# Optimization experiments

Hardware: AMD Instinct MI355X
Metric: run time of the kernel (lower is better)

## Reference

```python
import jax, jax.numpy as jnp
import numpy as np

K = 100
TEMPERATURE = 0.1


def setup_inputs() -> dict:
    key = jax.random.key(0)
    k1, k2 = jax.random.split(key)
    x = jax.random.normal(k1, (8, 128, 60, 60), dtype=jnp.float32)
    W = jax.random.normal(k2, (128, 2 * K), dtype=jnp.float32) * 0.02  # torch Linear(k*2, d_model).weight
    b = jnp.zeros((128,), dtype=jnp.float32)
    return {"x": x, "W": W, "b": b}


def reference(x, W, b):
    x0, x1 = jnp.split(x, 2, axis=0)
    n, c, h, w = x0.shape
    hw = h * w
    # n c h w -> n (h w) c
    f0 = jnp.transpose(x0.reshape(n, c, hw), (0, 2, 1))
    f1 = jnp.transpose(x1.reshape(n, c, hw), (0, 2, 1))
    # (f0/sqrt(c)) @ (f1/sqrt(c))^T / T  ==  f0 @ f1^T / (c*T)
    sm = jnp.einsum('nld,nsd->nls', f0, f1) / (c * TEMPERATURE)
    cm = (jax.nn.softmax(sm, axis=1) * jax.nn.softmax(sm, axis=2)).reshape(n, hw * hw)
    _, topi = jax.lax.top_k(cm, K)  # (n, K)
    qindex = topi // hw
    rindex = topi % hw
    coords0 = jnp.stack([qindex % w, qindex // w], axis=-1).astype(jnp.float32) / w  # (n, K, 2) as (x, y)
    coords1 = jnp.stack([rindex % w, rindex // w], axis=-1).astype(jnp.float32) / w
    # create_meshgrid(h, w, normalized=False): (1, h*w, 2) with (x, y), row-major
    gy, gx = jnp.meshgrid(jnp.arange(h), jnp.arange(w), indexing='ij')
    grid = jnp.stack([gx, gy], axis=-1).reshape(1, hw, 2).astype(jnp.float32) / w
    offsets0 = grid[:, :, None, :] - coords0[:, None, :, :]  # (n, hw, K, 2)
    offsets1 = grid[:, :, None, :] - coords1[:, None, :, :]
    emb0 = offsets0.reshape(n, hw, 2 * K) @ W.T + b  # (n, hw, d_model)
    emb1 = offsets1.reshape(n, hw, 2 * K) @ W.T + b
    f0 = f0 + emb0
    f1 = f1 + emb1
    f = jnp.concatenate([f0, f1], axis=0)  # (2n, hw, d)
    # n (h w) d -> n d h w
    return jnp.transpose(f, (0, 2, 1)).reshape(2 * n, c, h, w)
```

## Files before the change

### kernel.cpp

```cpp
#include <hip/hip_runtime.h>

#define HW 3600
#define PADR 3712
#define NF4 900
#define CAP 16384
#define KSEL 100
#define NT 58
typedef unsigned long long U64;

using short8   = __attribute__((ext_vector_type(8))) short;
using float4v  = __attribute__((ext_vector_type(4))) float;
using float16v = __attribute__((ext_vector_type(16))) float;

__device__ __forceinline__ unsigned monof(float f) {
    unsigned b = __float_as_uint(f);
    return (b & 0x80000000u) ? ~b : (b | 0x80000000u);
}
__device__ __forceinline__ float unmonof(unsigned m) {
    return __uint_as_float((m & 0x80000000u) ? (m ^ 0x80000000u) : ~m);
}
__device__ __forceinline__ unsigned short f2bf(float f) {
    unsigned b = __float_as_uint(f);
    return (unsigned short)((b + 0x7FFFu + ((b >> 16) & 1u)) >> 16);
}
__device__ __forceinline__ float bf2f(unsigned short h) {
    return __uint_as_float(((unsigned)h) << 16);
}
__device__ __forceinline__ void async16(const void* g, void* l) {
    __builtin_amdgcn_global_load_lds((const __attribute__((address_space(1))) void*)g,
                                     (__attribute__((address_space(3))) void*)l, 16, 0, 0);
}


__global__ __launch_bounds__(256) void conv_k(
    const float* __restrict__ x,
    unsigned short* __restrict__ hiT, unsigned short* __restrict__ loT)
{
    int b = blockIdx.z, l0 = blockIdx.x * 64, d0 = blockIdx.y * 64;
    __shared__ float t[64][65];
    int tid = threadIdx.x;
#pragma unroll
    for (int r = 0; r < 4; r++) {
        int idx = tid + 256 * r;
        int d = idx >> 4, lq = idx & 15;
        int l = l0 + lq * 4;
        const float* src = x + ((size_t)b * 128 + d0 + d) * HW;
        float4 v;
        if (l + 3 < HW) v = *(const float4*)(src + l);
        else {
            v.x = (l     < HW) ? src[l]     : 0.f;
            v.y = (l + 1 < HW) ? src[l + 1] : 0.f;
            v.z = (l + 2 < HW) ? src[l + 2] : 0.f;
            v.w = (l + 3 < HW) ? src[l + 3] : 0.f;
        }
        t[lq * 4 + 0][d] = v.x; t[lq * 4 + 1][d] = v.y;
        t[lq * 4 + 2][d] = v.z; t[lq * 4 + 3][d] = v.w;
    }
    __syncthreads();
    const int rblk = l0 >> 7;
#pragma unroll
    for (int r = 0; r < 2; r++) {
        int idx = tid + 256 * r;
        int l = idx & 63, dq = idx >> 6;
        unsigned hp[4], lp[4];
#pragma unroll
        for (int j = 0; j < 4; j++) {
            float f0 = t[l][dq * 8 + 2 * j], f1 = t[l][dq * 8 + 2 * j + 1];
            unsigned short h0 = f2bf(f0), h1 = f2bf(f1);
            unsigned short g0 = f2bf(f0 - bf2f(h0)), g1 = f2bf(f1 - bf2f(h1));
            hp[j] = (unsigned)h0 | ((unsigned)h1 << 16);
            lp[j] = (unsigned)g0 | ((unsigned)g1 << 16);
        }
        size_t o = ((size_t)(b * 29 + rblk) * 16 + (d0 >> 3) + dq) * 1024
                 + (size_t)((l0 + l) & 127) * 8;
        *(uint4*)(hiT + o) = make_uint4(hp[0], hp[1], hp[2], hp[3]);
        *(uint4*)(loT + o) = make_uint4(lp[0], lp[1], lp[2], lp[3]);
    }
}

__global__ __launch_bounds__(256) void gemm_mfma_k(
    const unsigned short* __restrict__ hiT, const unsigned short* __restrict__ loT,
    float* __restrict__ den_row, float* __restrict__ den_col,
    float* __restrict__ maxvt)
{
    const int batch = blockIdx.z, bx = blockIdx.x, by = blockIdx.y;
    __shared__ __align__(16) unsigned short stage[4][4][128][8];
    __shared__ float rowsumS[128], colsumS[128];

    const int tid = threadIdx.x;
    const int lane = tid & 63, w = tid >> 6;
    const int wr = w >> 1, wc = w & 1;
    const int l31 = lane & 31, h = lane >> 5;

    if (tid < 128) { rowsumS[tid] = 0.f; colsumS[tid] = 0.f; }

    const unsigned short* psrc = (w == 0) ? hiT : (w == 1) ? loT : (w == 2) ? hiT : loT;
    const int bsel = (w < 2) ? batch : batch + 4;
    const int rblk = (w < 2) ? by : bx;
    const size_t cbase = ((size_t)(bsel * 29 + rblk) * 16) * 1024;

    float16v acc[2][2];
#pragma unroll
    for (int i = 0; i < 2; i++)
#pragma unroll
        for (int j = 0; j < 2; j++) acc[i][j] = (float16v)(0.f);

    for (int k0 = 0; k0 < 128; k0 += 32) {
#pragma unroll
        for (int i = 0; i < 8; i++) {
            int kb = i >> 1, half = i & 1;
            const unsigned short* g = psrc + cbase + (size_t)((k0 >> 3) + kb) * 1024
                                    + (half << 9) + lane * 8;
            async16(g, &stage[w][kb][half << 6][0]);
        }
        __syncthreads();
#pragma unroll
        for (int j = 0; j < 2; j++) {
            int kb = j * 2 + h;
            short8 ah[2], al[2], bh[2], bl[2];
#pragma unroll
            for (int t = 0; t < 2; t++) {
                ah[t] = *(const short8*)&stage[0][kb][wr * 64 + t * 32 + l31][0];
                al[t] = *(const short8*)&stage[1][kb][wr * 64 + t * 32 + l31][0];
                bh[t] = *(const short8*)&stage[2][kb][wc * 64 + t * 32 + l31][0];
                bl[t] = *(const short8*)&stage[3][kb][wc * 64 + t * 32 + l31][0];
            }
#pragma unroll
            for (int mt = 0; mt < 2; mt++)
#pragma unroll
                for (int nt = 0; nt < 2; nt++) {
                    acc[mt][nt] = __builtin_amdgcn_mfma_f32_32x32x16_bf16(ah[mt], bh[nt], acc[mt][nt], 0, 0, 0);
                    acc[mt][nt] = __builtin_amdgcn_mfma_f32_32x32x16_bf16(ah[mt], bl[nt], acc[mt][nt], 0, 0, 0);
                    acc[mt][nt] = __builtin_amdgcn_mfma_f32_32x32x16_bf16(al[mt], bh[nt], acc[mt][nt], 0, 0, 0);
                }
        }
        __syncthreads();
    }

    const float scale = 0.078125f;
    float cs[2] = {0.f, 0.f};
    const int ct = bx * 2 + wc;
#pragma unroll
    for (int mt = 0; mt < 2; mt++) {
#pragma unroll
        for (int reg = 0; reg < 16; reg++) {
            int rloc = (reg & 3) + 8 * (reg >> 2) + 4 * h;
            int row128 = wr * 64 + mt * 32 + rloc;
            int l = by * 128 + row128;
            bool lv = (l < HW);
            float rs = 0.f, mx = -3.4e38f;
#pragma unroll
            for (int nt = 0; nt < 2; nt++) {
                int s = bx * 128 + wc * 64 + nt * 32 + l31;
                float v = acc[mt][nt][reg] * scale;
                if (s < HW) {
                    float e = __expf(v);
                    rs += e;
                    if (lv) cs[nt] += e;
                    mx = fmaxf(mx, v);
                }
            }
#pragma unroll
            for (int off = 1; off < 32; off <<= 1) {
                rs += __shfl_xor(rs, off);
                mx = fmaxf(mx, __shfl_xor(mx, off));
            }
            if (l31 == 0) {
                atomicAdd(&rowsumS[row128], rs);
                if (lv) maxvt[((size_t)batch * NT + ct) * PADR + l] = mx;
            }
        }
    }
#pragma unroll
    for (int nt = 0; nt < 2; nt++) {
        cs[nt] += __shfl_xor(cs[nt], 32);
        if (h == 0) atomicAdd(&colsumS[wc * 64 + nt * 32 + l31], cs[nt]);
    }
    __syncthreads();
    if (tid < 128) {
        int l = by * 128 + tid;
        if (l < HW) atomicAdd(&den_row[(size_t)batch * HW + l], rowsumS[tid]);
        int s = bx * 128 + tid;
        if (s < HW) atomicAdd(&den_col[(size_t)batch * HW + s], colsumS[tid]);
    }
}

__global__ __launch_bounds__(256) void logs_k(
    const float* __restrict__ den, float* __restrict__ lnD)
{
    int i = blockIdx.x * 256 + threadIdx.x;
    if (i < 28800) lnD[i] = __logf(den[i]);
}

__global__ __launch_bounds__(64) void tilestat_k(
    const float* __restrict__ lnDc, float* __restrict__ minlnc, float* __restrict__ maxlnc)
{
    int t = blockIdx.x, b = blockIdx.z, tid = threadIdx.x;
    int j = t * 64 + tid;
    float v = (j < HW) ? lnDc[(size_t)b * HW + j] : 0.f;
    float mn = (j < HW) ? v : 3.4e38f;
    float mx = (j < HW) ? v : -3.4e38f;
#pragma unroll
    for (int off = 1; off < 64; off <<= 1) {
        mn = fminf(mn, __shfl_xor(mn, off));
        mx = fmaxf(mx, __shfl_xor(mx, off));
    }
    if (tid == 0) {
        if (mx == -3.4e38f) { mx = 1e30f; mn = 1e30f; }
        minlnc[b * NT + t] = mn;
        maxlnc[b * NT + t] = mx;
    }
}

__global__ __launch_bounds__(256) void keylb_k(
    const float* __restrict__ maxvt, const float* __restrict__ lnDr,
    const float* __restrict__ maxlnc, float* __restrict__ keylb)
{
    int b = blockIdx.z, j = blockIdx.x * 256 + threadIdx.x;
    __shared__ float mls[NT];
    if (threadIdx.x < NT) mls[threadIdx.x] = maxlnc[b * NT + threadIdx.x];
    __syncthreads();
    if (j >= HW) return;
    float best = -3.4e38f;
#pragma unroll 2
    for (int t = 0; t < NT; t++) {
        float v = maxvt[((size_t)b * NT + t) * PADR + j];
        best = fmaxf(best, 2.0f * v - mls[t]);
    }
    keylb[(size_t)b * HW + j] = best - lnDr[(size_t)b * HW + j];
}

__global__ __launch_bounds__(256) void tau_k(
    const float* __restrict__ keylb, float* __restrict__ tau)
{
    const int b = blockIdx.z, tid = threadIdx.x;
    __shared__ unsigned keyS[HW];
    __shared__ unsigned hist[4096];
    __shared__ unsigned pc[256];
    __shared__ int b1S, c1S, b2S, lcnt;
    __shared__ unsigned bestS;
    __shared__ unsigned list[1024];

    for (int i = tid; i < 4096; i += 256) hist[i] = 0u;
    if (tid == 0) { lcnt = 0; bestS = 0u; }
    __syncthreads();
    for (int i = tid; i < HW; i += 256) {
        unsigned k = monof(keylb[(size_t)b * HW + i]);
        keyS[i] = k;
        atomicAdd(&hist[k >> 20], 1u);
    }
    __syncthreads();
    { unsigned s = 0; for (int j = 0; j < 16; j++) s += hist[tid * 16 + j]; pc[tid] = s; }
    __syncthreads();
    if (tid == 0) {
        unsigned cum = 0; int cs_ = 255;
        for (; cs_ > 0; cs_--) { if (cum + pc[cs_] >= (unsigned)KSEL) break; cum += pc[cs_]; }
        int bb = cs_ * 16 + 15;
        for (; bb > cs_ * 16; bb--) { if (cum + hist[bb] >= (unsigned)KSEL) break; cum += hist[bb]; }
        b1S = bb; c1S = (int)cum;
    }
    __syncthreads();
    int b1 = b1S;
    for (int i = tid; i < 4096; i += 256) hist[i] = 0u;
    __syncthreads();
    for (int i = tid; i < HW; i += 256) {
        unsigned k = keyS[i];
        if ((int)(k >> 20) == b1) atomicAdd(&hist[(k >> 8) & 4095], 1u);
    }
    __syncthreads();
    { unsigned s = 0; for (int j = 0; j < 16; j++) s += hist[tid * 16 + j]; pc[tid] = s; }
    __syncthreads();
    if (tid == 0) {
        unsigned cum = (unsigned)c1S; int cs_ = 255;
        for (; cs_ > 0; cs_--) { if (cum + pc[cs_] >= (unsigned)KSEL) break; cum += pc[cs_]; }
        int bb = cs_ * 16 + 15;
        for (; bb > cs_ * 16; bb--) { if (cum + hist[bb] >= (unsigned)KSEL) break; cum += hist[bb]; }
        b2S = bb;
    }
    __syncthreads();
    int b2 = b2S;
    for (int i = tid; i < HW; i += 256) {
        unsigned k = keyS[i]; int hb = (int)(k >> 20);
        if (hb > b1 || (hb == b1 && (int)((k >> 8) & 4095) >= b2)) {
            int p = atomicAdd(&lcnt, 1);
            if (p < 1024) list[p] = k;
        }
    }
    __syncthreads();
    int L = lcnt; if (L > 1024) L = 1024;
    for (int i = tid; i < L; i += 256) {
        unsigned e = list[i]; int c = 0;
        for (int j = 0; j < L; j++) c += (list[j] >= e) ? 1 : 0;
        if (c >= KSEL) atomicMax(&bestS, e);
    }
    __syncthreads();
    if (tid == 0) tau[b] = unmonof(bestS) - 3e-4f;
}

__global__ __launch_bounds__(256) void pairs_k(
    const float* __restrict__ maxvt, const float* __restrict__ lnDr,
    const float* __restrict__ minlnc, const float* __restrict__ tau,
    int* __restrict__ pairrows, int* __restrict__ paircnt)
{
    const int batch = blockIdx.z, t = blockIdx.x;
    const float tv = tau[batch] - 3e-4f;
    const float ml = minlnc[batch * NT + t];
    const float* mv = maxvt + ((size_t)batch * NT + t) * PADR;
    const float* ldr = lnDr + (size_t)batch * HW;
    int* pr = pairrows + ((size_t)batch * NT + t) * PADR;
    for (int r = threadIdx.x; r < HW; r += 256) {
        float b = 2.0f * mv[r] - ldr[r] - ml;
        if (b >= tv) {
            int p = atomicAdd(&paircnt[batch * NT + t], 1);
            pr[p] = r;
        }
    }
}

__global__ __launch_bounds__(256) void recollect_k(
    const unsigned short* __restrict__ hiT, const unsigned short* __restrict__ loT,
    const float* __restrict__ lnDr, const float* __restrict__ lnDc,
    const float* __restrict__ tau, const int* __restrict__ pairrows,
    const int* __restrict__ paircnt, uint2* __restrict__ cand,
    int* __restrict__ cnt)
{
    const int t = blockIdx.x, batch = blockIdx.y;
    const int pc = paircnt[batch * NT + t];
    if (pc == 0) return;
    const float tv = tau[batch];
    const int* pr = pairrows + ((size_t)batch * NT + t) * PADR;

    const unsigned short* Ah = hiT + (size_t)batch * PADR * 128;
    const unsigned short* Al = loT + (size_t)batch * PADR * 128;
    const unsigned short* Bh = hiT + (size_t)(batch + 4) * PADR * 128;
    const unsigned short* Bl = loT + (size_t)(batch + 4) * PADR * 128;

    const int tid = threadIdx.x;
    const int lane = tid & 63, w = tid >> 6;
    const int m = lane & 15, q = lane >> 4;
    const float scale = 0.078125f;

    for (int g = w; g * 16 < pc; g += 4) {
        int pi = g * 16 + m;
        int rowv = (pi < pc) ? pr[pi] : HW;
        float ldrv = (pi < pc) ? lnDr[(size_t)batch * HW + rowv] : 0.f;
        size_t arow = ((size_t)(rowv >> 7) * 16) * 1024 + (size_t)(rowv & 127) * 8;

        float4v acc[4];
#pragma unroll
        for (int i = 0; i < 4; i++) acc[i] = (float4v){0.f, 0.f, 0.f, 0.f};
#pragma unroll
        for (int k0 = 0; k0 < 128; k0 += 32) {
            int kb = (k0 >> 3) + q;
            short8 ah = *(const short8*)(Ah + arow + (size_t)kb * 1024);
            short8 al = *(const short8*)(Al + arow + (size_t)kb * 1024);
#pragma unroll
            for (int nt = 0; nt < 4; nt++) {
                int c = t * 64 + nt * 16 + m;
                size_t brow = ((size_t)(c >> 7) * 16 + kb) * 1024 + (size_t)(c & 127) * 8;
                short8 bh = *(const short8*)(Bh + brow);
                short8 bl = *(const short8*)(Bl + brow);
                acc[nt] = __builtin_amdgcn_mfma_f32_16x16x32_bf16(ah, bh, acc[nt], 0, 0, 0);
                acc[nt] = __builtin_amdgcn_mfma_f32_16x16x32_bf16(ah, bl, acc[nt], 0, 0, 0);
                acc[nt] = __builtin_amdgcn_mfma_f32_16x16x32_bf16(al, bh, acc[nt], 0, 0, 0);
            }
        }
#pragma unroll
        for (int nt = 0; nt < 4; nt++) {
            int c = t * 64 + nt * 16 + m;
            if (c >= HW) continue;
            float ldc = lnDc[(size_t)batch * HW + c];
#pragma unroll
            for (int r = 0; r < 4; r++) {
                int ri = q * 4 + r;
                if (g * 16 + ri >= pc) continue;
                int rowo = __shfl(rowv, ri);
                float ldro = __shfl(ldrv, ri);
                float v = acc[nt][r] * scale;
                float tt = 2.0f * v - ldro - ldc;
                if (tt >= tv) {
                    int p = atomicAdd(&cnt[batch], 1);
                    if (p < CAP)
                        cand[(size_t)batch * CAP + p] =
                            make_uint2(monof(tt), (unsigned)(rowo * HW + c));
                }
            }
        }
    }
}

__global__ __launch_bounds__(256) void select_k(
    const uint2* __restrict__ cand, const int* __restrict__ cnt,
    const float* __restrict__ W,
    float* __restrict__ C0, float* __restrict__ C1,
    float* __restrict__ Sx, float* __restrict__ Sy)
{
    const int batch = blockIdx.z, tid = threadIdx.x;
    const uint2* cb = cand + (size_t)batch * CAP;
    int M = cnt[batch]; if (M > CAP) M = CAP;

    __shared__ unsigned hist[4096];
    __shared__ unsigned pc[256];
    __shared__ int b1S, c1S, b2S, lcnt;
    __shared__ U64 list[512];
    __shared__ int topiS[KSEL];
    __shared__ float cx0S[KSEL], cy0S[KSEL], cx1S[KSEL], cy1S[KSEL];

    for (int i = tid; i < 4096; i += 256) hist[i] = 0u;
    if (tid == 0) lcnt = 0;
    __syncthreads();
    for (int i = tid; i < M; i += 256) atomicAdd(&hist[cb[i].x >> 20], 1u);
    __syncthreads();
    { unsigned s = 0; for (int j = 0; j < 16; j++) s += hist[tid * 16 + j]; pc[tid] = s; }
    __syncthreads();
    if (tid == 0) {
        unsigned cum = 0; int cs_ = 255;
        for (; cs_ > 0; cs_--) { if (cum + pc[cs_] >= (unsigned)KSEL) break; cum += pc[cs_]; }
        int bb = cs_ * 16 + 15;
        for (; bb > cs_ * 16; bb--) { if (cum + hist[bb] >= (unsigned)KSEL) break; cum += hist[bb]; }
        b1S = bb; c1S = (int)cum;
    }
    __syncthreads();
    int b1 = b1S;
    for (int i = tid; i < 4096; i += 256) hist[i] = 0u;
    __syncthreads();
    for (int i = tid; i < M; i += 256) {
        unsigned k = cb[i].x;
        if ((int)(k >> 20) == b1) atomicAdd(&hist[(k >> 8) & 4095], 1u);
    }
    __syncthreads();
    { unsigned s = 0; for (int j = 0; j < 16; j++) s += hist[tid * 16 + j]; pc[tid] = s; }
    __syncthreads();
    if (tid == 0) {
        unsigned cum = (unsigned)c1S; int cs_ = 255;
        for (; cs_ > 0; cs_--) { if (cum + pc[cs_] >= (unsigned)KSEL) break; cum += pc[cs_]; }
        int bb = cs_ * 16 + 15;
        for (; bb > cs_ * 16; bb--) { if (cum + hist[bb] >= (unsigned)KSEL) break; cum += hist[bb]; }
        b2S = bb;
    }
    __syncthreads();
    int b2 = b2S;
    for (int i = tid; i < M; i += 256) {
        uint2 e = cb[i];
        int hb = (int)(e.x >> 20);
        if (hb > b1 || (hb == b1 && (int)((e.x >> 8) & 4095) >= b2)) {
            int p = atomicAdd(&lcnt, 1);
            if (p < 512) list[p] = ((U64)e.x << 32) | (unsigned)(~e.y);
        }
    }
    __syncthreads();
    int L = lcnt; if (L > 512) L = 512;
    for (int i = tid; i < L; i += 256) {
        U64 e = list[i]; int r = 0;
        for (int j = 0; j < L; j++) r += (list[j] > e) ? 1 : 0;
        if (r < KSEL) topiS[r] = (int)(~(unsigned)(e & 0xffffffffu));
    }
    __syncthreads();

    if (tid < KSEL) {
        int idx = topiS[tid];
        int qq = idx / HW, rr = idx - qq * HW;
        cx0S[tid] = (float)(qq % 60) / 60.0f;
        cy0S[tid] = (float)(qq / 60) / 60.0f;
        cx1S[tid] = (float)(rr % 60) / 60.0f;
        cy1S[tid] = (float)(rr / 60) / 60.0f;
    }
    __syncthreads();
    if (tid < 128) {
        const float* wr_ = W + tid * 200;
        float c0 = 0.f, c1 = 0.f, sx = 0.f, sy = 0.f;
        for (int k = 0; k < KSEL; k++) {
            float wx = wr_[2 * k], wy = wr_[2 * k + 1];
            c0 += cx0S[k] * wx + cy0S[k] * wy;
            c1 += cx1S[k] * wx + cy1S[k] * wy;
            sx += wx; sy += wy;
        }
        C0[batch * 128 + tid] = c0;
        C1[batch * 128 + tid] = c1;
        if (batch == 0) { Sx[tid] = sx; Sy[tid] = sy; }
    }
}

__global__ __launch_bounds__(256) void final_k(
    const float* __restrict__ x, const float* __restrict__ bias,
    const float* __restrict__ C0, const float* __restrict__ C1,
    const float* __restrict__ Sx, const float* __restrict__ Sy,
    float* __restrict__ out)
{
    int bd = blockIdx.x;
    int b = bd >> 7, d = bd & 127;
    float cst = bias[d] - ((b < 4) ? C0[b * 128 + d] : C1[(b - 4) * 128 + d]);
    float sx = Sx[d], sy = Sy[d];
    const float4* xin = (const float4*)(x + (size_t)bd * HW);
    float4* o4 = (float4*)(out + (size_t)bd * HW);
    for (int f = threadIdx.x; f < NF4; f += 256) {
        float4 v = xin[f];
        int p0 = f * 4;
        float gy = (float)(p0 / 60) / 60.0f;
        float gxb = (float)(p0 % 60);
        float add = cst + gy * sy;
        v.x += add + ((gxb       ) / 60.0f) * sx;
        v.y += add + ((gxb + 1.f) / 60.0f) * sx;
        v.z += add + ((gxb + 2.f) / 60.0f) * sx;
        v.w += add + ((gxb + 3.f) / 60.0f) * sx;
        o4[f] = v;
    }
}

extern "C" void kernel_launch(void* const* d_in, const int* in_sizes, int n_in,
                              void* d_out, int out_size, void* d_ws, size_t ws_size,
                              hipStream_t stream)
{
    const float* x    = (const float*)d_in[0];
    const float* W    = (const float*)d_in[1];
    const float* bias = (const float*)d_in[2];
    float* out = (float*)d_out;

    char* ws = (char*)d_ws;
    float*    den     = (float*)(ws + 0);
    float*    den_row = den;
    float*    den_col = (float*)(ws + 57600);
    float*    lnD     = (float*)(ws + 115200);
    float*    lnDr    = lnD;
    float*    lnDc    = (float*)(ws + 172800);
    int*      cnt     = (int*)  (ws + 230400);
    float*    tau     = (float*)(ws + 230416);
    float*    minlnc  = (float*)(ws + 230432);
    float*    maxlnc  = (float*)(ws + 231360);
    int*      paircnt = (int*)  (ws + 232288);
    float*    keylb   = (float*)(ws + 233216);
    float*    C0      = (float*)(ws + 290816);
    float*    C1      = (float*)(ws + 292864);
    float*    Sx      = (float*)(ws + 294912);
    float*    Sy      = (float*)(ws + 295424);
    uint2*    cand    = (uint2*)(ws + 295936);
    int*      pairrows= (int*)  (ws + 820224);
    float*    maxvt   = (float*)(ws + 4264960);
    unsigned short* hiT = (unsigned short*)(ws + 7709696);
    unsigned short* loT = (unsigned short*)(ws + 15311872);

    hipMemsetAsync(ws, 0, 115200, stream);
    hipMemsetAsync(ws + 230400, 0, 32, stream);
    hipMemsetAsync(ws + 232288, 0, 928, stream);

    conv_k     <<<dim3(58, 2, 8),  256, 0, stream>>>(x, hiT, loT);
    gemm_mfma_k<<<dim3(29, 29, 4), 256, 0, stream>>>(hiT, loT, den_row, den_col, maxvt);
    logs_k     <<<dim3(113),       256, 0, stream>>>(den, lnD);
    tilestat_k <<<dim3(NT, 1, 4),   64, 0, stream>>>(lnDc, minlnc, maxlnc);
    keylb_k    <<<dim3(15, 1, 4),  256, 0, stream>>>(maxvt, lnDr, maxlnc, keylb);
    tau_k      <<<dim3(1, 1, 4),   256, 0, stream>>>(keylb, tau);
    pairs_k    <<<dim3(NT, 1, 4),  256, 0, stream>>>(maxvt, lnDr, minlnc, tau, pairrows, paircnt);
    recollect_k<<<dim3(NT, 4),     256, 0, stream>>>(hiT, loT, lnDr, lnDc, tau, pairrows, paircnt, cand, cnt);
    select_k   <<<dim3(1, 1, 4),   256, 0, stream>>>(cand, cnt, W, C0, C1, Sx, Sy);
    final_k    <<<dim3(1024),      256, 0, stream>>>(x, bias, C0, C1, Sx, Sy, out);
}
```

Before: 263.0 us.

## Rework GEMM epilogue via LDS transpose and fuse small stat kernels

The GEMM epilogue now writes exp values and scaled maxima into a per-wave padded LDS tile and reduces rows by having each lane read its own row. This replaces the shuffle-butterfly reductions and the shared-memory atomics, and interior tiles skip the bounds checks. The log, tile-stat and key kernels are merged into one stat kernel, and the pair-listing kernel is folded into recollect using shared memory. This cuts kernel launches, memsets and intermediate global buffers, but recomputes logs redundantly in every block.

After: 229.9 us. 1.14x faster.

```diff
diff --git a/kernel.cpp b/kernel.cpp
--- a/kernel.cpp
+++ b/kernel.cpp
@@ -84,15 +84,13 @@
     float* __restrict__ maxvt)
 {
     const int batch = blockIdx.z, bx = blockIdx.x, by = blockIdx.y;
-    __shared__ __align__(16) unsigned short stage[4][4][128][8];
-    __shared__ float rowsumS[128], colsumS[128];
+    __shared__ __align__(16) unsigned char smem[34816];
+    unsigned short (*stage)[4][128][8] = (unsigned short (*)[4][128][8])smem;
 
     const int tid = threadIdx.x;
     const int lane = tid & 63, w = tid >> 6;
     const int wr = w >> 1, wc = w & 1;
     const int l31 = lane & 31, h = lane >> 5;
-
-    if (tid < 128) { rowsumS[tid] = 0.f; colsumS[tid] = 0.f; }
 
     const unsigned short* psrc = (w == 0) ? hiT : (w == 1) ? loT : (w == 2) ? hiT : loT;
     const int bsel = (w < 2) ? batch : batch + 4;
@@ -138,96 +136,91 @@
     }
 
     const float scale = 0.078125f;
-    float cs[2] = {0.f, 0.f};
+    float* T = ((float*)smem) + w * (64 * 34);
+    const bool interior = (bx < 28) && (by < 28);
+    const int col0 = bx * 128 + wc * 64 + l31;
+    const bool c0v = interior || (col0 < HW);
+    const bool c1v = interior || (col0 + 32 < HW);
+    float cs0 = 0.f, cs1 = 0.f;
+
+#pragma unroll
+    for (int mt = 0; mt < 2; mt++)
+#pragma unroll
+        for (int reg = 0; reg < 16; reg++) {
+            float v0 = acc[mt][0][reg] * scale;
+            float v1 = acc[mt][1][reg] * scale;
+            float e0 = c0v ? __expf(v0) : 0.f;
+            float e1 = c1v ? __expf(v1) : 0.f;
+            int row64 = mt * 32 + (reg & 3) + 8 * (reg >> 2) + 4 * h;
+            bool rv = interior || (by * 128 + wr * 64 + row64 < HW);
+            if (rv) { cs0 += e0; cs1 += e1; }
+            T[row64 * 34 + l31] = e0 + e1;
+        }
+    __asm__ __volatile__("s_waitcnt lgkmcnt(0)" ::: "memory");
+    float rsum = 0.f;
+#pragma unroll
+    for (int i = 0; i < 16; i++) {
+        float2 p = *(const float2*)&T[lane * 34 + 2 * i];
+        rsum += p.x + p.y;
+    }
+    __asm__ __volatile__("s_waitcnt lgkmcnt(0)" ::: "memory");
+    const int lrow = by * 128 + wr * 64 + lane;
+    const bool rowv = interior || (lrow < HW);
+    if (rowv) atomicAdd(&den_row[(size_t)batch * HW + lrow], rsum);
+
+#pragma unroll
+    for (int mt = 0; mt < 2; mt++)
+#pragma unroll
+        for (int reg = 0; reg < 16; reg++) {
+            float m0 = c0v ? acc[mt][0][reg] : -3.4e38f;
+            float m1 = c1v ? acc[mt][1][reg] : -3.4e38f;
+            int row64 = mt * 32 + (reg & 3) + 8 * (reg >> 2) + 4 * h;
+            T[row64 * 34 + l31] = fmaxf(m0, m1) * scale;
+        }
+    __asm__ __volatile__("s_waitcnt lgkmcnt(0)" ::: "memory");
+    float rmax = -3.4e38f;
+#pragma unroll
+    for (int i = 0; i < 16; i++) {
+        float2 p = *(const float2*)&T[lane * 34 + 2 * i];
+        rmax = fmaxf(rmax, fmaxf(p.x, p.y));
+    }
     const int ct = bx * 2 + wc;
-#pragma unroll
-    for (int mt = 0; mt < 2; mt++) {
-#pragma unroll
-        for (int reg = 0; reg < 16; reg++) {
-            int rloc = (reg & 3) + 8 * (reg >> 2) + 4 * h;
-            int row128 = wr * 64 + mt * 32 + rloc;
-            int l = by * 128 + row128;
-            bool lv = (l < HW);
-            float rs = 0.f, mx = -3.4e38f;
-#pragma unroll
-            for (int nt = 0; nt < 2; nt++) {
-                int s = bx * 128 + wc * 64 + nt * 32 + l31;
-                float v = acc[mt][nt][reg] * scale;
-                if (s < HW) {
-                    float e = __expf(v);
-                    rs += e;
-                    if (lv) cs[nt] += e;
-                    mx = fmaxf(mx, v);
-                }
-            }
-#pragma unroll
-            for (int off = 1; off < 32; off <<= 1) {
-                rs += __shfl_xor(rs, off);
-                mx = fmaxf(mx, __shfl_xor(mx, off));
-            }
-            if (l31 == 0) {
-                atomicAdd(&rowsumS[row128], rs);
-                if (lv) maxvt[((size_t)batch * NT + ct) * PADR + l] = mx;
-            }
-        }
-    }
-#pragma unroll
-    for (int nt = 0; nt < 2; nt++) {
-        cs[nt] += __shfl_xor(cs[nt], 32);
-        if (h == 0) atomicAdd(&colsumS[wc * 64 + nt * 32 + l31], cs[nt]);
-    }
-    __syncthreads();
-    if (tid < 128) {
-        int l = by * 128 + tid;
-        if (l < HW) atomicAdd(&den_row[(size_t)batch * HW + l], rowsumS[tid]);
-        int s = bx * 128 + tid;
-        if (s < HW) atomicAdd(&den_col[(size_t)batch * HW + s], colsumS[tid]);
-    }
-}
-
-__global__ __launch_bounds__(256) void logs_k(
-    const float* __restrict__ den, float* __restrict__ lnD)
-{
-    int i = blockIdx.x * 256 + threadIdx.x;
-    if (i < 28800) lnD[i] = __logf(den[i]);
-}
-
-__global__ __launch_bounds__(64) void tilestat_k(
-    const float* __restrict__ lnDc, float* __restrict__ minlnc, float* __restrict__ maxlnc)
-{
-    int t = blockIdx.x, b = blockIdx.z, tid = threadIdx.x;
-    int j = t * 64 + tid;
-    float v = (j < HW) ? lnDc[(size_t)b * HW + j] : 0.f;
-    float mn = (j < HW) ? v : 3.4e38f;
-    float mx = (j < HW) ? v : -3.4e38f;
-#pragma unroll
-    for (int off = 1; off < 64; off <<= 1) {
-        mn = fminf(mn, __shfl_xor(mn, off));
-        mx = fmaxf(mx, __shfl_xor(mx, off));
-    }
-    if (tid == 0) {
-        if (mx == -3.4e38f) { mx = 1e30f; mn = 1e30f; }
-        minlnc[b * NT + t] = mn;
-        maxlnc[b * NT + t] = mx;
-    }
-}
-
-__global__ __launch_bounds__(256) void keylb_k(
-    const float* __restrict__ maxvt, const float* __restrict__ lnDr,
-    const float* __restrict__ maxlnc, float* __restrict__ keylb)
-{
-    int b = blockIdx.z, j = blockIdx.x * 256 + threadIdx.x;
-    __shared__ float mls[NT];
-    if (threadIdx.x < NT) mls[threadIdx.x] = maxlnc[b * NT + threadIdx.x];
-    __syncthreads();
-    if (j >= HW) return;
-    float best = -3.4e38f;
+    if (rowv) maxvt[((size_t)batch * NT + ct) * PADR + lrow] = rmax;
+
+    cs0 += __shfl_xor(cs0, 32);
+    cs1 += __shfl_xor(cs1, 32);
+    if (h == 0) {
+        if (c0v) atomicAdd(&den_col[(size_t)batch * HW + col0], cs0);
+        if (c1v) atomicAdd(&den_col[(size_t)batch * HW + col0 + 32], cs1);
+    }
+}
+
+__global__ __launch_bounds__(256) void stat_k(
+    const float* __restrict__ den_row, const float* __restrict__ den_col,
+    const float* __restrict__ maxvt, float* __restrict__ keylb)
+{
+    const int b = blockIdx.z, tid = threadIdx.x;
+    __shared__ float lncS[HW];
+    __shared__ float mlsS[NT];
+    for (int i = tid; i < HW; i += 256)
+        lncS[i] = __logf(den_col[(size_t)b * HW + i]);
+    __syncthreads();
+    if (tid < NT) {
+        float mx = -3.4e38f;
+        int s0 = tid * 64, s1 = s0 + 64; if (s1 > HW) s1 = HW;
+        for (int s = s0; s < s1; s++) mx = fmaxf(mx, lncS[s]);
+        if (s0 >= HW) mx = 1e30f;
+        mlsS[tid] = mx;
+    }
+    __syncthreads();
+    int j = blockIdx.x * 240 + tid;
+    if (tid < 240 && j < HW) {
+        float best = -3.4e38f;
 #pragma unroll 2
-    for (int t = 0; t < NT; t++) {
-        float v = maxvt[((size_t)b * NT + t) * PADR + j];
-        best = fmaxf(best, 2.0f * v - mls[t]);
-    }
-    keylb[(size_t)b * HW + j] = best - lnDr[(size_t)b * HW + j];
+        for (int t = 0; t < NT; t++)
+            best = fmaxf(best, 2.0f * maxvt[((size_t)b * NT + t) * PADR + j] - mlsS[t]);
+        keylb[(size_t)b * HW + j] = best - __logf(den_row[(size_t)b * HW + j]);
+    }
 }
 
 __global__ __launch_bounds__(256) void tau_k(
@@ -297,54 +290,62 @@
     if (tid == 0) tau[b] = unmonof(bestS) - 3e-4f;
 }
 
-__global__ __launch_bounds__(256) void pairs_k(
-    const float* __restrict__ maxvt, const float* __restrict__ lnDr,
-    const float* __restrict__ minlnc, const float* __restrict__ tau,
-    int* __restrict__ pairrows, int* __restrict__ paircnt)
-{
-    const int batch = blockIdx.z, t = blockIdx.x;
-    const float tv = tau[batch] - 3e-4f;
-    const float ml = minlnc[batch * NT + t];
-    const float* mv = maxvt + ((size_t)batch * NT + t) * PADR;
-    const float* ldr = lnDr + (size_t)batch * HW;
-    int* pr = pairrows + ((size_t)batch * NT + t) * PADR;
-    for (int r = threadIdx.x; r < HW; r += 256) {
-        float b = 2.0f * mv[r] - ldr[r] - ml;
-        if (b >= tv) {
-            int p = atomicAdd(&paircnt[batch * NT + t], 1);
-            pr[p] = r;
-        }
-    }
-}
-
 __global__ __launch_bounds__(256) void recollect_k(
     const unsigned short* __restrict__ hiT, const unsigned short* __restrict__ loT,
-    const float* __restrict__ lnDr, const float* __restrict__ lnDc,
-    const float* __restrict__ tau, const int* __restrict__ pairrows,
-    const int* __restrict__ paircnt, uint2* __restrict__ cand,
-    int* __restrict__ cnt)
+    const float* __restrict__ den_row, const float* __restrict__ den_col,
+    const float* __restrict__ maxvt, const float* __restrict__ tau,
+    uint2* __restrict__ cand, int* __restrict__ cnt)
 {
     const int t = blockIdx.x, batch = blockIdx.y;
-    const int pc = paircnt[batch * NT + t];
+    const int tid = threadIdx.x;
+    __shared__ float lnrS[HW];
+    __shared__ float lncS[64];
+    __shared__ int prS[HW];
+    __shared__ int pcS;
+    __shared__ float mnlS;
+
+    if (tid < 64) {
+        int c = t * 64 + tid;
+        float lc = (c < HW) ? __logf(den_col[(size_t)batch * HW + c]) : 1e30f;
+        lncS[tid] = lc;
+        float mn = lc;
+#pragma unroll
+        for (int off = 1; off < 64; off <<= 1) mn = fminf(mn, __shfl_xor(mn, off));
+        if (tid == 0) mnlS = mn;
+    }
+    for (int r = tid; r < HW; r += 256)
+        lnrS[r] = __logf(den_row[(size_t)batch * HW + r]);
+    if (tid == 0) pcS = 0;
+    __syncthreads();
+
+    const float tv = tau[batch];
+    const float tvm = tv - 3e-4f;
+    const float mnl = mnlS;
+    const float* mv = maxvt + ((size_t)batch * NT + t) * PADR;
+    for (int r = tid; r < HW; r += 256) {
+        float bnd = 2.0f * mv[r] - lnrS[r] - mnl;
+        if (bnd >= tvm) {
+            int p = atomicAdd(&pcS, 1);
+            prS[p] = r;
+        }
+    }
+    __syncthreads();
+    const int pc = pcS;
     if (pc == 0) return;
-    const float tv = tau[batch];
-    const int* pr = pairrows + ((size_t)batch * NT + t) * PADR;
-
-    const unsigned short* Ah = hiT + (size_t)batch * PADR * 128;
-    const unsigned short* Al = loT + (size_t)batch * PADR * 128;
-    const unsigned short* Bh = hiT + (size_t)(batch + 4) * PADR * 128;
-    const unsigned short* Bl = loT + (size_t)(batch + 4) * PADR * 128;
-
-    const int tid = threadIdx.x;
+
+    const unsigned short* Ah = hiT + 0;
+    const unsigned short* Al = loT + 0;
     const int lane = tid & 63, w = tid >> 6;
     const int m = lane & 15, q = lane >> 4;
     const float scale = 0.078125f;
+    const size_t abase = (size_t)batch * PADR * 128;
+    const size_t bbase = (size_t)(batch + 4) * PADR * 128;
 
     for (int g = w; g * 16 < pc; g += 4) {
         int pi = g * 16 + m;
-        int rowv = (pi < pc) ? pr[pi] : HW;
-        float ldrv = (pi < pc) ? lnDr[(size_t)batch * HW + rowv] : 0.f;
-        size_t arow = ((size_t)(rowv >> 7) * 16) * 1024 + (size_t)(rowv & 127) * 8;
+        int rowv = (pi < pc) ? prS[pi] : HW;
+        float ldrv = (pi < pc) ? lnrS[rowv] : 0.f;
+        size_t arow = abase + ((size_t)(rowv >> 7) * 16) * 1024 + (size_t)(rowv & 127) * 8;
 
         float4v acc[4];
 #pragma unroll
@@ -357,9 +358,9 @@
 #pragma unroll
             for (int nt = 0; nt < 4; nt++) {
                 int c = t * 64 + nt * 16 + m;
-                size_t brow = ((size_t)(c >> 7) * 16 + kb) * 1024 + (size_t)(c & 127) * 8;
-                short8 bh = *(const short8*)(Bh + brow);
-                short8 bl = *(const short8*)(Bl + brow);
+                size_t brow = bbase + ((size_t)(c >> 7) * 16 + kb) * 1024 + (size_t)(c & 127) * 8;
+                short8 bh = *(const short8*)(hiT + brow);
+                short8 bl = *(const short8*)(loT + brow);
                 acc[nt] = __builtin_amdgcn_mfma_f32_16x16x32_bf16(ah, bh, acc[nt], 0, 0, 0);
                 acc[nt] = __builtin_amdgcn_mfma_f32_16x16x32_bf16(ah, bl, acc[nt], 0, 0, 0);
                 acc[nt] = __builtin_amdgcn_mfma_f32_16x16x32_bf16(al, bh, acc[nt], 0, 0, 0);
@@ -369,7 +370,7 @@
         for (int nt = 0; nt < 4; nt++) {
             int c = t * 64 + nt * 16 + m;
             if (c >= HW) continue;
-            float ldc = lnDc[(size_t)batch * HW + c];
+            float ldc = lncS[nt * 16 + m];
 #pragma unroll
             for (int r = 0; r < 4; r++) {
                 int ri = q * 4 + r;
@@ -517,40 +518,27 @@
     float* out = (float*)d_out;
 
     char* ws = (char*)d_ws;
-    float*    den     = (float*)(ws + 0);
-    float*    den_row = den;
+    float*    den_row = (float*)(ws + 0);
     float*    den_col = (float*)(ws + 57600);
-    float*    lnD     = (float*)(ws + 115200);
-    float*    lnDr    = lnD;
-    float*    lnDc    = (float*)(ws + 172800);
-    int*      cnt     = (int*)  (ws + 230400);
-    float*    tau     = (float*)(ws + 230416);
-    float*    minlnc  = (float*)(ws + 230432);
-    float*    maxlnc  = (float*)(ws + 231360);
-    int*      paircnt = (int*)  (ws + 232288);
-    float*    keylb   = (float*)(ws + 233216);
-    float*    C0      = (float*)(ws + 290816);
-    float*    C1      = (float*)(ws + 292864);
-    float*    Sx      = (float*)(ws + 294912);
-    float*    Sy      = (float*)(ws + 295424);
-    uint2*    cand    = (uint2*)(ws + 295936);
-    int*      pairrows= (int*)  (ws + 820224);
-    float*    maxvt   = (float*)(ws + 4264960);
-    unsigned short* hiT = (unsigned short*)(ws + 7709696);
-    unsigned short* loT = (unsigned short*)(ws + 15311872);
-
-    hipMemsetAsync(ws, 0, 115200, stream);
-    hipMemsetAsync(ws + 230400, 0, 32, stream);
-    hipMemsetAsync(ws + 232288, 0, 928, stream);
+    int*      cnt     = (int*)  (ws + 115200);
+    float*    tau     = (float*)(ws + 115216);
+    float*    keylb   = (float*)(ws + 115264);
+    float*    C0      = (float*)(ws + 172864);
+    float*    C1      = (float*)(ws + 174912);
+    float*    Sx      = (float*)(ws + 176960);
+    float*    Sy      = (float*)(ws + 177472);
+    uint2*    cand    = (uint2*)(ws + 178048);
+    float*    maxvt   = (float*)(ws + 702336);
+    unsigned short* hiT = (unsigned short*)(ws + 4147072);
+    unsigned short* loT = (unsigned short*)(ws + 11749248);
+
+    hipMemsetAsync(ws, 0, 115232, stream);
 
     conv_k     <<<dim3(58, 2, 8),  256, 0, stream>>>(x, hiT, loT);
     gemm_mfma_k<<<dim3(29, 29, 4), 256, 0, stream>>>(hiT, loT, den_row, den_col, maxvt);
-    logs_k     <<<dim3(113),       256, 0, stream>>>(den, lnD);
-    tilestat_k <<<dim3(NT, 1, 4),   64, 0, stream>>>(lnDc, minlnc, maxlnc);
-    keylb_k    <<<dim3(15, 1, 4),  256, 0, stream>>>(maxvt, lnDr, maxlnc, keylb);
+    stat_k     <<<dim3(15, 1, 4),  256, 0, stream>>>(den_row, den_col, maxvt, keylb);
     tau_k      <<<dim3(1, 1, 4),   256, 0, stream>>>(keylb, tau);
-    pairs_k    <<<dim3(NT, 1, 4),  256, 0, stream>>>(maxvt, lnDr, minlnc, tau, pairrows, paircnt);
-    recollect_k<<<dim3(NT, 4),     256, 0, stream>>>(hiT, loT, lnDr, lnDc, tau, pairrows, paircnt, cand, cnt);
+    recollect_k<<<dim3(NT, 4),     256, 0, stream>>>(hiT, loT, den_row, den_col, maxvt, tau, cand, cnt);
     select_k   <<<dim3(1, 1, 4),   256, 0, stream>>>(cand, cnt, W, C0, C1, Sx, Sy);
     final_k    <<<dim3(1024),      256, 0, stream>>>(x, bias, C0, C1, Sx, Sy, out);
 }
```
